# Kernel tuning notes

Hardware: AMD Instinct MI355X
Metric: run time of the kernel (lower is better)

Reference implementation:

```python
import jax, jax.numpy as jnp
import numpy as np

B, N, C = 2, 2048, 768
H = 12
HD = C // H  # 64


def setup_inputs() -> dict:
    key = jax.random.key(0)
    ks = jax.random.split(key, 6)
    s = 0.02
    x = jax.random.normal(ks[0], (B, N, C), dtype=jnp.float32)
    xpos = jnp.arange(B * N, dtype=jnp.int64).reshape(B, N) % N
    W_qkv = jax.random.normal(ks[1], (3 * C, C), dtype=jnp.float32) * s
    b_qkv = jnp.zeros((3 * C,), dtype=jnp.float32)
    W_proj = jax.random.normal(ks[2], (C, C), dtype=jnp.float32) * s
    b_proj = jnp.zeros((C,), dtype=jnp.float32)
    return {"x": x, "xpos": xpos, "W_qkv": W_qkv, "b_qkv": b_qkv,
            "W_proj": W_proj, "b_proj": b_proj}


def reference(x, xpos, W_qkv, b_qkv, W_proj, b_proj):
    # rope is None in this configuration -> xpos is unused, matching torch module.
    Bx, Nx, Cx = x.shape
    scale = (Cx // H) ** -0.5
    qkv = x @ W_qkv.T + b_qkv                     # [B, N, 3C]
    qkv = qkv.reshape(Bx, Nx, 3, H, HD)
    q = jnp.einsum('bnhd->bhnd', qkv[:, :, 0])    # [B, H, N, HD]
    k = jnp.einsum('bnhd->bhnd', qkv[:, :, 1])
    v = jnp.einsum('bnhd->bhnd', qkv[:, :, 2])
    attn = jnp.einsum('bhnd,bhmd->bhnm', q, k) * scale  # [B, H, N, N]
    attn = jax.nn.softmax(attn, axis=-1)
    out = jnp.einsum('bhnm,bhmd->bhnd', attn, v)  # [B, H, N, HD]
    out = jnp.einsum('bhnd->bnhd', out).reshape(Bx, Nx, Cx)
    return out @ W_proj.T + b_proj
```

## Files before the change

kernel.cpp:

```cpp
#include <hip/hip_runtime.h>
#include <hip/hip_bf16.h>


typedef _Float16 half8 __attribute__((ext_vector_type(8)));
typedef _Float16 half4_t __attribute__((ext_vector_type(4)));
typedef float floatx4 __attribute__((ext_vector_type(4)));

#define LDA 72
#define LDP 72
#define SCALE_LOG2E 0.1803368801111204f

constexpr int XH_OFF    = 0;
constexpr int WQKV_OFF  = XH_OFF + 4096 * 768;
constexpr int WPROJ_OFF = WQKV_OFF + 2304 * 768;
constexpr int QK_OFF    = WPROJ_OFF + 768 * 768;
constexpr int VTH_OFF   = QK_OFF + 4096 * 1536;

__global__ __launch_bounds__(256) void cvt_all(const float* __restrict__ x,
                                               const float* __restrict__ wqkv,
                                               const float* __restrict__ wproj,
                                               _Float16* __restrict__ ws) {
  constexpr int n1 = 4096 * 768 / 4;
  constexpr int n2 = 2304 * 768 / 4;
  int i = blockIdx.x * 256 + threadIdx.x;
  const float* src; _Float16* dst; int j;
  if (i < n1)           { src = x;     dst = ws + XH_OFF;    j = i; }
  else if (i < n1 + n2) { src = wqkv;  dst = ws + WQKV_OFF;  j = i - n1; }
  else                  { src = wproj; dst = ws + WPROJ_OFF; j = i - n1 - n2; }
  floatx4 f = *(const floatx4*)(src + 4 * j);
  half4_t h;
  h[0] = (_Float16)f[0]; h[1] = (_Float16)f[1];
  h[2] = (_Float16)f[2]; h[3] = (_Float16)f[3];
  *(half4_t*)(dst + 4 * j) = h;
}

__global__ __launch_bounds__(256) void qkv_gemm(const _Float16* __restrict__ xh,
                                                const _Float16* __restrict__ wh,
                                                const float* __restrict__ bias,
                                                _Float16* __restrict__ qkh,
                                                _Float16* __restrict__ vth) {
  __shared__ __align__(16) _Float16 sA[128 * LDA];
  __shared__ __align__(16) _Float16 sB[128 * LDA];
  const int tid = threadIdx.x;
  const int nblk = blockIdx.x % 18, mblk = blockIdx.x / 18;
  const int lane = tid & 63, w = tid >> 6;
  const int lane15 = lane & 15, quad = lane >> 4;
  const int wm = w >> 1, wn = w & 1;
  const int chunk = tid & 7, rbase = tid >> 3;

  const int Abase = mblk * 128 * 768;
  const int Bbase = nblk * 128 * 768;

  floatx4 acc[4][4];
#pragma unroll
  for (int mt = 0; mt < 4; ++mt)
#pragma unroll
    for (int nt = 0; nt < 4; ++nt) acc[mt][nt] = (floatx4){0.f, 0.f, 0.f, 0.f};

  for (int kt = 0; kt < 12; ++kt) {
    half8 ta[4], tb[4];
#pragma unroll
    for (int i = 0; i < 4; ++i) {
      int row = rbase + 32 * i;
      ta[i] = *(const half8*)(xh + Abase + row * 768 + kt * 64 + chunk * 8);
      tb[i] = *(const half8*)(wh + Bbase + row * 768 + kt * 64 + chunk * 8);
    }
    if (kt) __syncthreads();
#pragma unroll
    for (int i = 0; i < 4; ++i) {
      int row = rbase + 32 * i;
      *(half8*)(sA + row * LDA + chunk * 8) = ta[i];
      *(half8*)(sB + row * LDA + chunk * 8) = tb[i];
    }
    __syncthreads();
#pragma unroll
    for (int ks = 0; ks < 2; ++ks) {
      half8 af[4], bf[4];
#pragma unroll
      for (int mt = 0; mt < 4; ++mt)
        af[mt] = *(const half8*)(sA + (wm * 64 + mt * 16 + lane15) * LDA + ks * 32 + quad * 8);
#pragma unroll
      for (int nt = 0; nt < 4; ++nt)
        bf[nt] = *(const half8*)(sB + (wn * 64 + nt * 16 + lane15) * LDA + ks * 32 + quad * 8);
#pragma unroll
      for (int mt = 0; mt < 4; ++mt)
#pragma unroll
        for (int nt = 0; nt < 4; ++nt)
          acc[mt][nt] = __builtin_amdgcn_mfma_f32_16x16x32_f16(af[mt], bf[nt], acc[mt][nt], 0, 0, 0);
    }
  }

  const int mbase = mblk * 128 + wm * 64;
  const int nbase = nblk * 128 + wn * 64;
#pragma unroll
  for (int nt = 0; nt < 4; ++nt) {
    int cbase = nbase + nt * 16;
    float bv = bias[cbase + lane15];
    if (cbase < 1536) {
      int col = cbase + lane15;
#pragma unroll
      for (int mt = 0; mt < 4; ++mt)
#pragma unroll
        for (int r = 0; r < 4; ++r) {
          int token = mbase + mt * 16 + quad * 4 + r;
          qkh[token * 1536 + col] = (_Float16)(acc[mt][nt][r] + bv);
        }
    } else {
      int dcol = cbase - 1536 + lane15;
      int h = dcol >> 6, d = dcol & 63;
#pragma unroll
      for (int mt = 0; mt < 4; ++mt) {
        int tok0 = mbase + mt * 16 + quad * 4;
        int b = tok0 >> 11, n0 = tok0 & 2047;
        int bh = b * 12 + h;
        half4_t hv;
#pragma unroll
        for (int r = 0; r < 4; ++r) hv[r] = (_Float16)(acc[mt][nt][r] + bv);
        *(half4_t*)(vth + (bh * 64 + d) * 2048 + n0) = hv;
      }
    }
  }
}

__global__ __launch_bounds__(256) void attn_fused(const _Float16* __restrict__ qkh,
                                                  const _Float16* __restrict__ vth,
                                                  _Float16* __restrict__ aoh) {
  __shared__ __align__(16) _Float16 sK[64 * LDA];
  __shared__ __align__(16) _Float16 sVT[64 * LDA];
  __shared__ __align__(16) _Float16 sP[4 * 16 * LDP];
  const int tid = threadIdx.x;
  const int bx = blockIdx.x;
  const int bh = bx % 24, qt = bx / 24;
  const int b = bh / 12, h = bh % 12;
  const int lane = tid & 63, w = tid >> 6;
  const int lane15 = lane & 15, quad = lane >> 4;
  const int chunk = tid & 7, rbase = tid >> 3;
  _Float16* sPw = sP + w * 16 * LDP;

  const int qkbase = b * 2048 * 1536 + h * 64;
  const int qrow = qt * 64 + w * 16 + lane15;
  half8 qa0 = *(const half8*)(qkh + qkbase + qrow * 1536 + quad * 8);
  half8 qa1 = *(const half8*)(qkh + qkbase + qrow * 1536 + 32 + quad * 8);

  const _Float16* kptr = qkh + qkbase + 768;
  const _Float16* vptr = vth + bh * 64 * 2048;

  floatx4 O[4];
#pragma unroll
  for (int dt = 0; dt < 4; ++dt) O[dt] = (floatx4){0.f, 0.f, 0.f, 0.f};
  float mrow = -3.0e38f, lrow = 0.f;

  for (int kt = 0; kt < 32; ++kt) {
    half8 tk[2], tv[2];
#pragma unroll
    for (int i = 0; i < 2; ++i) {
      int row = rbase + 32 * i;
      tk[i] = *(const half8*)(kptr + (kt * 64 + row) * 1536 + chunk * 8);
      tv[i] = *(const half8*)(vptr + row * 2048 + kt * 64 + chunk * 8);
    }
    if (kt) __syncthreads();
#pragma unroll
    for (int i = 0; i < 2; ++i) {
      int row = rbase + 32 * i;
      *(half8*)(sK + row * LDA + chunk * 8) = tk[i];
      *(half8*)(sVT + row * LDA + chunk * 8) = tv[i];
    }
    __syncthreads();

    floatx4 s[4];
#pragma unroll
    for (int nt = 0; nt < 4; ++nt) {
      half8 kf0 = *(const half8*)(sK + (nt * 16 + lane15) * LDA + quad * 8);
      half8 kf1 = *(const half8*)(sK + (nt * 16 + lane15) * LDA + 32 + quad * 8);
      floatx4 a = (floatx4){0.f, 0.f, 0.f, 0.f};
      a = __builtin_amdgcn_mfma_f32_16x16x32_f16(kf0, qa0, a, 0, 0, 0);
      a = __builtin_amdgcn_mfma_f32_16x16x32_f16(kf1, qa1, a, 0, 0, 0);
#pragma unroll
      for (int r = 0; r < 4; ++r) a[r] *= SCALE_LOG2E;
      s[nt] = a;
    }

    float tmax = s[0][0];
#pragma unroll
    for (int nt = 0; nt < 4; ++nt)
#pragma unroll
      for (int r = 0; r < 4; ++r) tmax = fmaxf(tmax, s[nt][r]);
    tmax = fmaxf(tmax, __shfl_xor(tmax, 16, 64));
    tmax = fmaxf(tmax, __shfl_xor(tmax, 32, 64));
    float mnew = fmaxf(mrow, tmax);
    float alpha = exp2f(mrow - mnew);
    float rsum = 0.f;
#pragma unroll
    for (int nt = 0; nt < 4; ++nt)
#pragma unroll
      for (int r = 0; r < 4; ++r) {
        float p = exp2f(s[nt][r] - mnew);
        s[nt][r] = p;
        rsum += p;
      }
    rsum += __shfl_xor(rsum, 16, 64);
    rsum += __shfl_xor(rsum, 32, 64);
    lrow = lrow * alpha + rsum;
    mrow = mnew;

    float ar[4];
#pragma unroll
    for (int r = 0; r < 4; ++r) ar[r] = __shfl(alpha, 4 * quad + r, 64);
#pragma unroll
    for (int dt = 0; dt < 4; ++dt)
#pragma unroll
      for (int r = 0; r < 4; ++r) O[dt][r] *= ar[r];

#pragma unroll
    for (int nt = 0; nt < 4; ++nt) {
      half4_t hp;
#pragma unroll
      for (int r = 0; r < 4; ++r) hp[r] = (_Float16)s[nt][r];
      *(half4_t*)(sPw + lane15 * LDP + nt * 16 + quad * 4) = hp;
    }
    asm volatile("s_waitcnt lgkmcnt(0)" ::: "memory");

#pragma unroll
    for (int kk = 0; kk < 2; ++kk) {
      half8 pa = *(const half8*)(sPw + lane15 * LDP + kk * 32 + quad * 8);
#pragma unroll
      for (int dt = 0; dt < 4; ++dt) {
        half8 vb = *(const half8*)(sVT + (dt * 16 + lane15) * LDA + kk * 32 + quad * 8);
        O[dt] = __builtin_amdgcn_mfma_f32_16x16x32_f16(pa, vb, O[dt], 0, 0, 0);
      }
    }
  }

  float inv = 1.0f / lrow;
  float ir[4];
#pragma unroll
  for (int r = 0; r < 4; ++r) ir[r] = __shfl(inv, 4 * quad + r, 64);
#pragma unroll
  for (int dt = 0; dt < 4; ++dt)
#pragma unroll
    for (int r = 0; r < 4; ++r) {
      int tok = qt * 64 + w * 16 + quad * 4 + r;
      aoh[(b * 2048 + tok) * 768 + h * 64 + dt * 16 + lane15] = (_Float16)(O[dt][r] * ir[r]);
    }
}

__global__ __launch_bounds__(256) void proj_gemm(const _Float16* __restrict__ ah,
                                                 const _Float16* __restrict__ wh,
                                                 const float* __restrict__ bias,
                                                 float* __restrict__ out) {
  __shared__ __align__(16) _Float16 sA[128 * LDA];
  __shared__ __align__(16) _Float16 sB[128 * LDA];
  const int tid = threadIdx.x;
  const int nblk = blockIdx.x % 6, mblk = blockIdx.x / 6;
  const int lane = tid & 63, w = tid >> 6;
  const int lane15 = lane & 15, quad = lane >> 4;
  const int wm = w >> 1, wn = w & 1;
  const int chunk = tid & 7, rbase = tid >> 3;

  const int Abase = mblk * 128 * 768;
  const int Bbase = nblk * 128 * 768;

  floatx4 acc[4][4];
#pragma unroll
  for (int mt = 0; mt < 4; ++mt)
#pragma unroll
    for (int nt = 0; nt < 4; ++nt) acc[mt][nt] = (floatx4){0.f, 0.f, 0.f, 0.f};

  for (int kt = 0; kt < 12; ++kt) {
    half8 ta[4], tb[4];
#pragma unroll
    for (int i = 0; i < 4; ++i) {
      int row = rbase + 32 * i;
      ta[i] = *(const half8*)(ah + Abase + row * 768 + kt * 64 + chunk * 8);
      tb[i] = *(const half8*)(wh + Bbase + row * 768 + kt * 64 + chunk * 8);
    }
    if (kt) __syncthreads();
#pragma unroll
    for (int i = 0; i < 4; ++i) {
      int row = rbase + 32 * i;
      *(half8*)(sA + row * LDA + chunk * 8) = ta[i];
      *(half8*)(sB + row * LDA + chunk * 8) = tb[i];
    }
    __syncthreads();
#pragma unroll
    for (int ks = 0; ks < 2; ++ks) {
      half8 af[4], bf[4];
#pragma unroll
      for (int mt = 0; mt < 4; ++mt)
        af[mt] = *(const half8*)(sA + (wm * 64 + mt * 16 + lane15) * LDA + ks * 32 + quad * 8);
#pragma unroll
      for (int nt = 0; nt < 4; ++nt)
        bf[nt] = *(const half8*)(sB + (wn * 64 + nt * 16 + lane15) * LDA + ks * 32 + quad * 8);
#pragma unroll
      for (int mt = 0; mt < 4; ++mt)
#pragma unroll
        for (int nt = 0; nt < 4; ++nt)
          acc[mt][nt] = __builtin_amdgcn_mfma_f32_16x16x32_f16(af[mt], bf[nt], acc[mt][nt], 0, 0, 0);
    }
  }

  const int mbase = mblk * 128 + wm * 64;
  const int nbase = nblk * 128 + wn * 64;
#pragma unroll
  for (int nt = 0; nt < 4; ++nt) {
    int col = nbase + nt * 16 + lane15;
    float bv = bias[col];
#pragma unroll
    for (int mt = 0; mt < 4; ++mt)
#pragma unroll
      for (int r = 0; r < 4; ++r) {
        int token = mbase + mt * 16 + quad * 4 + r;
        out[token * 768 + col] = acc[mt][nt][r] + bv;
      }
  }
}

extern "C" void kernel_launch(void* const* d_in, const int* in_sizes, int n_in,
                              void* d_out, int out_size, void* d_ws, size_t ws_size,
                              hipStream_t stream) {
  const float* x     = (const float*)d_in[0];
  const float* wqkv  = (const float*)d_in[2];
  const float* bqkv  = (const float*)d_in[3];
  const float* wproj = (const float*)d_in[4];
  const float* bproj = (const float*)d_in[5];
  float* out = (float*)d_out;

  _Float16* ws = (_Float16*)d_ws;
  _Float16* xh     = ws + XH_OFF;
  _Float16* wqkvh  = ws + WQKV_OFF;
  _Float16* wprojh = ws + WPROJ_OFF;
  _Float16* qkh    = ws + QK_OFF;
  _Float16* vth    = ws + VTH_OFF;
  _Float16* aoh    = xh;

  constexpr int total_v4 = (4096 * 768 + 2304 * 768 + 768 * 768) / 4;
  cvt_all<<<total_v4 / 256, 256, 0, stream>>>(x, wqkv, wproj, ws);
  qkv_gemm<<<32 * 18, 256, 0, stream>>>(xh, wqkvh, bqkv, qkh, vth);
  attn_fused<<<24 * 32, 256, 0, stream>>>(qkh, vth, aoh);
  proj_gemm<<<32 * 6, 256, 0, stream>>>(aoh, wprojh, bproj, out);
}
```

Baseline: 191.0 us.

## Use direct global-to-LDS loads in GEMMs, fold softmax scale into Q, lazy rescale

Both GEMM kernels now stage tiles with global_load_lds 16-byte direct copies instead of going through registers, which drops the LDS padding (stride 64 instead of 72). The softmax scale times log2e is folded into Q in the QKV epilogue, removing the per-score multiply in attention. The online softmax now rescales O and l only when some row's max increases, skipping exp and shuffles on other iterations. The unpadded LDS layout may cause bank conflicts on fragment reads, and the direct loads are not double-buffered.

After: 192.3 us. Within noise of the previous version (+0.7%).

```diff
diff --git a/kernel.cpp b/kernel.cpp
--- a/kernel.cpp
+++ b/kernel.cpp
@@ -15,6 +15,12 @@
 constexpr int WPROJ_OFF = WQKV_OFF + 2304 * 768;
 constexpr int QK_OFF    = WPROJ_OFF + 768 * 768;
 constexpr int VTH_OFF   = QK_OFF + 4096 * 1536;
+
+__device__ __forceinline__ void gl16(const _Float16* g, _Float16* l) {
+  __builtin_amdgcn_global_load_lds(
+      (const __attribute__((address_space(1))) unsigned int*)g,
+      (__attribute__((address_space(3))) unsigned int*)l, 16, 0, 0);
+}
 
 __global__ __launch_bounds__(256) void cvt_all(const float* __restrict__ x,
                                                const float* __restrict__ wqkv,
@@ -39,17 +45,18 @@
                                                 const float* __restrict__ bias,
                                                 _Float16* __restrict__ qkh,
                                                 _Float16* __restrict__ vth) {
-  __shared__ __align__(16) _Float16 sA[128 * LDA];
-  __shared__ __align__(16) _Float16 sB[128 * LDA];
+  __shared__ __align__(16) _Float16 sA[128 * 64];
+  __shared__ __align__(16) _Float16 sB[128 * 64];
   const int tid = threadIdx.x;
   const int nblk = blockIdx.x % 18, mblk = blockIdx.x / 18;
   const int lane = tid & 63, w = tid >> 6;
   const int lane15 = lane & 15, quad = lane >> 4;
   const int wm = w >> 1, wn = w & 1;
-  const int chunk = tid & 7, rbase = tid >> 3;
+  const int lrow = lane >> 3, lchunk = lane & 7;
 
   const int Abase = mblk * 128 * 768;
   const int Bbase = nblk * 128 * 768;
+  const int r0 = w * 32;
 
   floatx4 acc[4][4];
 #pragma unroll
@@ -58,19 +65,12 @@
     for (int nt = 0; nt < 4; ++nt) acc[mt][nt] = (floatx4){0.f, 0.f, 0.f, 0.f};
 
   for (int kt = 0; kt < 12; ++kt) {
-    half8 ta[4], tb[4];
+    if (kt) __syncthreads();
 #pragma unroll
     for (int i = 0; i < 4; ++i) {
-      int row = rbase + 32 * i;
-      ta[i] = *(const half8*)(xh + Abase + row * 768 + kt * 64 + chunk * 8);
-      tb[i] = *(const half8*)(wh + Bbase + row * 768 + kt * 64 + chunk * 8);
-    }
-    if (kt) __syncthreads();
-#pragma unroll
-    for (int i = 0; i < 4; ++i) {
-      int row = rbase + 32 * i;
-      *(half8*)(sA + row * LDA + chunk * 8) = ta[i];
-      *(half8*)(sB + row * LDA + chunk * 8) = tb[i];
+      int row = r0 + 8 * i + lrow;
+      gl16(xh + Abase + row * 768 + kt * 64 + lchunk * 8, sA + (r0 + 8 * i) * 64);
+      gl16(wh + Bbase + row * 768 + kt * 64 + lchunk * 8, sB + (r0 + 8 * i) * 64);
     }
     __syncthreads();
 #pragma unroll
@@ -78,10 +78,10 @@
       half8 af[4], bf[4];
 #pragma unroll
       for (int mt = 0; mt < 4; ++mt)
-        af[mt] = *(const half8*)(sA + (wm * 64 + mt * 16 + lane15) * LDA + ks * 32 + quad * 8);
+        af[mt] = *(const half8*)(sA + (wm * 64 + mt * 16 + lane15) * 64 + ks * 32 + quad * 8);
 #pragma unroll
       for (int nt = 0; nt < 4; ++nt)
-        bf[nt] = *(const half8*)(sB + (wn * 64 + nt * 16 + lane15) * LDA + ks * 32 + quad * 8);
+        bf[nt] = *(const half8*)(sB + (wn * 64 + nt * 16 + lane15) * 64 + ks * 32 + quad * 8);
 #pragma unroll
       for (int mt = 0; mt < 4; ++mt)
 #pragma unroll
@@ -98,12 +98,13 @@
     float bv = bias[cbase + lane15];
     if (cbase < 1536) {
       int col = cbase + lane15;
+      float sc = (cbase < 768) ? SCALE_LOG2E : 1.0f;
 #pragma unroll
       for (int mt = 0; mt < 4; ++mt)
 #pragma unroll
         for (int r = 0; r < 4; ++r) {
           int token = mbase + mt * 16 + quad * 4 + r;
-          qkh[token * 1536 + col] = (_Float16)(acc[mt][nt][r] + bv);
+          qkh[token * 1536 + col] = (_Float16)((acc[mt][nt][r] + bv) * sc);
         }
     } else {
       int dcol = cbase - 1536 + lane15;
@@ -175,8 +176,6 @@
       floatx4 a = (floatx4){0.f, 0.f, 0.f, 0.f};
       a = __builtin_amdgcn_mfma_f32_16x16x32_f16(kf0, qa0, a, 0, 0, 0);
       a = __builtin_amdgcn_mfma_f32_16x16x32_f16(kf1, qa1, a, 0, 0, 0);
-#pragma unroll
-      for (int r = 0; r < 4; ++r) a[r] *= SCALE_LOG2E;
       s[nt] = a;
     }
 
@@ -187,29 +186,33 @@
       for (int r = 0; r < 4; ++r) tmax = fmaxf(tmax, s[nt][r]);
     tmax = fmaxf(tmax, __shfl_xor(tmax, 16, 64));
     tmax = fmaxf(tmax, __shfl_xor(tmax, 32, 64));
-    float mnew = fmaxf(mrow, tmax);
-    float alpha = exp2f(mrow - mnew);
+
+    if (__any(tmax > mrow)) {
+      float mnew = fmaxf(mrow, tmax);
+      float alpha = exp2f(mrow - mnew);
+      lrow *= alpha;
+      mrow = mnew;
+      float ar[4];
+#pragma unroll
+      for (int r = 0; r < 4; ++r) ar[r] = __shfl(alpha, 4 * quad + r, 64);
+#pragma unroll
+      for (int dt = 0; dt < 4; ++dt)
+#pragma unroll
+        for (int r = 0; r < 4; ++r) O[dt][r] *= ar[r];
+    }
+
     float rsum = 0.f;
 #pragma unroll
     for (int nt = 0; nt < 4; ++nt)
 #pragma unroll
       for (int r = 0; r < 4; ++r) {
-        float p = exp2f(s[nt][r] - mnew);
+        float p = exp2f(s[nt][r] - mrow);
         s[nt][r] = p;
         rsum += p;
       }
     rsum += __shfl_xor(rsum, 16, 64);
     rsum += __shfl_xor(rsum, 32, 64);
-    lrow = lrow * alpha + rsum;
-    mrow = mnew;
-
-    float ar[4];
-#pragma unroll
-    for (int r = 0; r < 4; ++r) ar[r] = __shfl(alpha, 4 * quad + r, 64);
-#pragma unroll
-    for (int dt = 0; dt < 4; ++dt)
-#pragma unroll
-      for (int r = 0; r < 4; ++r) O[dt][r] *= ar[r];
+    lrow += rsum;
 
 #pragma unroll
     for (int nt = 0; nt < 4; ++nt) {
@@ -248,17 +251,18 @@
                                                  const _Float16* __restrict__ wh,
                                                  const float* __restrict__ bias,
                                                  float* __restrict__ out) {
-  __shared__ __align__(16) _Float16 sA[128 * LDA];
-  __shared__ __align__(16) _Float16 sB[128 * LDA];
+  __shared__ __align__(16) _Float16 sA[128 * 64];
+  __shared__ __align__(16) _Float16 sB[128 * 64];
   const int tid = threadIdx.x;
   const int nblk = blockIdx.x % 6, mblk = blockIdx.x / 6;
   const int lane = tid & 63, w = tid >> 6;
   const int lane15 = lane & 15, quad = lane >> 4;
   const int wm = w >> 1, wn = w & 1;
-  const int chunk = tid & 7, rbase = tid >> 3;
+  const int lrow = lane >> 3, lchunk = lane & 7;
 
   const int Abase = mblk * 128 * 768;
   const int Bbase = nblk * 128 * 768;
+  const int r0 = w * 32;
 
   floatx4 acc[4][4];
 #pragma unroll
@@ -267,19 +271,12 @@
     for (int nt = 0; nt < 4; ++nt) acc[mt][nt] = (floatx4){0.f, 0.f, 0.f, 0.f};
 
   for (int kt = 0; kt < 12; ++kt) {
-    half8 ta[4], tb[4];
+    if (kt) __syncthreads();
 #pragma unroll
     for (int i = 0; i < 4; ++i) {
-      int row = rbase + 32 * i;
-      ta[i] = *(const half8*)(ah + Abase + row * 768 + kt * 64 + chunk * 8);
-      tb[i] = *(const half8*)(wh + Bbase + row * 768 + kt * 64 + chunk * 8);
-    }
-    if (kt) __syncthreads();
-#pragma unroll
-    for (int i = 0; i < 4; ++i) {
-      int row = rbase + 32 * i;
-      *(half8*)(sA + row * LDA + chunk * 8) = ta[i];
-      *(half8*)(sB + row * LDA + chunk * 8) = tb[i];
+      int row = r0 + 8 * i + lrow;
+      gl16(ah + Abase + row * 768 + kt * 64 + lchunk * 8, sA + (r0 + 8 * i) * 64);
+      gl16(wh + Bbase + row * 768 + kt * 64 + lchunk * 8, sB + (r0 + 8 * i) * 64);
     }
     __syncthreads();
 #pragma unroll
@@ -287,10 +284,10 @@
       half8 af[4], bf[4];
 #pragma unroll
       for (int mt = 0; mt < 4; ++mt)
-        af[mt] = *(const half8*)(sA + (wm * 64 + mt * 16 + lane15) * LDA + ks * 32 + quad * 8);
+        af[mt] = *(const half8*)(sA + (wm * 64 + mt * 16 + lane15) * 64 + ks * 32 + quad * 8);
 #pragma unroll
       for (int nt = 0; nt < 4; ++nt)
-        bf[nt] = *(const half8*)(sB + (wn * 64 + nt * 16 + lane15) * LDA + ks * 32 + quad * 8);
+        bf[nt] = *(const half8*)(sB + (wn * 64 + nt * 16 + lane15) * 64 + ks * 32 + quad * 8);
 #pragma unroll
       for (int mt = 0; mt < 4; ++mt)
 #pragma unroll
```
